# Kernel tuning notes

Hardware: AMD Instinct MI355X
Metric: run time of the kernel (lower is better)

Reference implementation:

```python
import jax, jax.numpy as jnp
import numpy as np

N_USER = 100000
M_ITEM = 50000
N_NODE = N_USER + M_ITEM
D = 64           # latent_dim
WD = D // 2      # word_emb_dim
FU = FI = 10     # padded feature-bag width
NUF = NIF = 30000
VOCAB = 20000
T = 8            # tokens per text source (name/comment/comment_list)
DNU = DNI = 10   # numeric feature dims
B = 2048         # seed batch
S = 20           # sampled neighbors per layer
L = 2            # num_layers


def setup_inputs() -> dict:
    key = jax.random.key(0)
    ks = jax.random.split(key, 26)
    f = lambda i, s: jax.random.normal(ks[i], s, jnp.float32) * 0.05
    ri = lambda i, s, hi: jax.random.randint(ks[i], s, 0, hi)
    return {
        # int (graph / lookup) inputs
        "seeds": ri(0, (B,), N_USER),
        "neigh1": ri(1, (B, S), N_NODE),
        "neigh2": ri(2, (B, S, S), N_NODE),
        "user_feat_idx": ri(3, (N_USER, FU), NUF),
        "item_feat_idx": ri(4, (M_ITEM, FI), NIF),
        "user_text_idx": ri(5, (N_USER, 3, T), VOCAB),
        "item_text_idx": ri(6, (M_ITEM, 3, T), VOCAB),
        # float tables / features
        "user_id_emb": f(7, (N_USER, D)),
        "item_id_emb": f(8, (M_ITEM, D)),
        "user_feat_emb": f(9, (NUF, D)),
        "item_feat_emb": f(10, (NIF, D)),
        "word_emb": f(11, (VOCAB, WD)),
        "user_word300": f(12, (N_USER, 300)),
        "item_word300": f(13, (M_ITEM, 300)),
        "item_sent768": f(14, (M_ITEM, 768)),
        "user_numeric": f(15, (N_USER, DNU)),
        "item_numeric": f(16, (M_ITEM, DNI)),
        # linears (stored as (in, out); y = x @ W + b)
        "Wnum_u": f(17, (DNU, D)), "bnum_u": jnp.zeros((D,), jnp.float32),
        "Wnum_i": f(18, (DNI, D)), "bnum_i": jnp.zeros((D,), jnp.float32),
        "Wproj_u": f(19, (int(D * 3.5) + 300, D)), "bproj_u": jnp.zeros((D,), jnp.float32),
        "Wproj_i": f(20, (int(D * 3.5) + 300 + 768, D)), "bproj_i": jnp.zeros((D,), jnp.float32),
        "W_w": f(21, (L, 2 * D, D)), "b_w": jnp.zeros((L, D), jnp.float32),
        "W_v": f(22, (L, D, D)), "b_v": jnp.zeros((L, D), jnp.float32),
    }


def _forward(user_id_emb, item_id_emb, user_feat_emb, item_feat_emb, word_emb,
             user_word300, item_word300, item_sent768, user_numeric, item_numeric,
             Wnum_u, bnum_u, Wnum_i, bnum_i, Wproj_u, bproj_u, Wproj_i, bproj_i,
             W_w, b_w, W_v, b_v,
             seeds, neigh1, neigh2, user_feat_idx, item_feat_idx,
             user_text_idx, item_text_idx):
    # --- multi-source node embeddings (get_text_embedding + proj + numeric) ---
    # text: mean-pool word embeddings per source, concat 3 sources -> 1.5*D
    u_text = word_emb[user_text_idx].mean(axis=2).reshape(N_USER, 3 * WD)
    i_text = word_emb[item_text_idx].mean(axis=2).reshape(M_ITEM, 3 * WD)
    # feature bags: mean-pooled embedding lookup
    u_feat = user_feat_emb[user_feat_idx].mean(axis=1)
    i_feat = item_feat_emb[item_feat_idx].mean(axis=1)
    u = (jnp.concatenate([user_id_emb, u_feat, u_text, user_word300], -1) @ Wproj_u
         + bproj_u + user_numeric @ Wnum_u + bnum_u)
    it = (jnp.concatenate([item_id_emb, i_feat, i_text, item_word300, item_sent768], -1) @ Wproj_i
          + bproj_i + item_numeric @ Wnum_i + bnum_i)
    x = jnp.concatenate([u, it], axis=0)  # [N_NODE, D], items offset by N_USER

    # --- neighbor-sampled GraphSAGE: h = W_l([self, mean(V_l(neigh))]) ---
    def sage(l, self_x, neigh_x, act):
        agg = (neigh_x @ W_v[l] + b_v[l]).mean(axis=-2)
        h = jnp.concatenate([self_x, agg], axis=-1) @ W_w[l] + b_w[l]
        return jax.nn.relu(h) if act else h

    x0 = x[seeds]        # [B, D]
    x1 = x[neigh1]       # [B, S, D]
    x2 = x[neigh2]       # [B, S, S, D]
    h1 = sage(0, x1, x2, True)   # layer-0 applied to 1-hop nodes
    h0 = sage(0, x0, x1, True)   # layer-0 applied to seeds
    out = sage(1, h0, h1, False)  # final layer, no activation
    return out  # [B, D]


def reference(seeds, neigh1, neigh2, user_feat_idx, item_feat_idx, user_text_idx,
              item_text_idx, user_id_emb, item_id_emb, user_feat_emb, item_feat_emb,
              word_emb, user_word300, item_word300, item_sent768, user_numeric,
              item_numeric, Wnum_u, bnum_u, Wnum_i, bnum_i, Wproj_u, bproj_u,
              Wproj_i, bproj_i, W_w, b_w, W_v, b_v):
    return _forward(user_id_emb, item_id_emb, user_feat_emb, item_feat_emb, word_emb,
                    user_word300, item_word300, item_sent768, user_numeric, item_numeric,
                    Wnum_u, bnum_u, Wnum_i, bnum_i, Wproj_u, bproj_u, Wproj_i, bproj_i,
                    W_w, b_w, W_v, b_v,
                    seeds, neigh1, neigh2, user_feat_idx, item_feat_idx,
                    user_text_idx, item_text_idx)
```

## Files before the change

kernel.cpp:

```cpp
#include <hip/hip_runtime.h>
#include <hip/hip_bf16.h>
#include <stdint.h>

#define N_USER 100000
#define M_ITEM 50000
#define N_NODE 150000
#define B_SEED 2048
#define S_NB 20
#define UBLK2 1563
#define IBLK2 782

typedef __bf16   bf16x8 __attribute__((ext_vector_type(8)));
typedef float    f32x4  __attribute__((ext_vector_type(4)));
typedef uint32_t u32x4  __attribute__((ext_vector_type(4)));

__device__ __forceinline__ uint16_t f2bf(float f) {
    uint32_t u = __float_as_uint(f);
    return (uint16_t)((u + 0x7FFFu + ((u >> 16) & 1u)) >> 16);
}
__device__ __forceinline__ uint32_t pk2(float a, float b) {
    __hip_bfloat162 h = __float22bfloat162_rn(make_float2(a, b));
    return *reinterpret_cast<uint32_t*>(&h);
}
__device__ __forceinline__ float bf2f(uint16_t u) {
    return __uint_as_float(((uint32_t)u) << 16);
}

union BF8 { bf16x8 v; uint32_t u[4]; uint2 d2[2]; };

__device__ __forceinline__ bf16x8 pack8v(f32x4 lo, f32x4 hi) {
    BF8 r;
    r.u[0] = pk2(lo[0], lo[1]); r.u[1] = pk2(lo[2], lo[3]);
    r.u[2] = pk2(hi[0], hi[1]); r.u[3] = pk2(hi[2], hi[3]);
    return r.v;
}
__device__ __forceinline__ bf16x8 ldf32x8_mask(const float* rowp, int base, int limit) {
    BF8 r;
#pragma unroll
    for (int h = 0; h < 4; ++h) {
        const int k0 = base + 2 * h;
        const float a = (k0     < limit) ? rowp[k0]     : 0.f;
        const float b = (k0 + 1 < limit) ? rowp[k0 + 1] : 0.f;
        r.u[h] = pk2(a, b);
    }
    return r.v;
}

__global__ void prep_kernel(const float* __restrict__ Wproj_u, const float* __restrict__ Wnum_u,
                            const float* __restrict__ Wproj_i, const float* __restrict__ Wnum_i,
                            const float* __restrict__ Wv0, const float* __restrict__ Ww0,
                            uint16_t* __restrict__ WTU, uint16_t* __restrict__ WTI,
                            uint16_t* __restrict__ WvT, uint16_t* __restrict__ WwT)
{
    const int idx = blockIdx.x * 256 + threadIdx.x;
    if (idx < 36864) {
        const int d = idx / 576, kp = idx - d * 576;
        float v = 0.f;
        if (kp < 160)      v = Wproj_u[(64 + kp) * 64 + d];
        else if (kp < 192) { const int j = kp - 160; if (j < 10)  v = Wnum_u[j * 64 + d]; }
        else if (kp < 256) v = Wproj_u[(kp - 192) * 64 + d];
        else               { const int j = kp - 256; if (j < 300) v = Wproj_u[(224 + j) * 64 + d]; }
        WTU[d * 576 + kp] = f2bf(v);
    } else if (idx < 122880) {
        const int i2 = idx - 36864;
        const int d = i2 / 1344, kp = i2 - d * 1344;
        float v = 0.f;
        if (kp < 160)      v = Wproj_i[(64 + kp) * 64 + d];
        else if (kp < 192) { const int j = kp - 160; if (j < 10)  v = Wnum_i[j * 64 + d]; }
        else if (kp < 256) v = Wproj_i[(kp - 192) * 64 + d];
        else if (kp < 576) { const int j = kp - 256; if (j < 300) v = Wproj_i[(224 + j) * 64 + d]; }
        else               { const int j = kp - 576; v = Wproj_i[(524 + j) * 64 + d]; }
        WTI[d * 1344 + kp] = f2bf(v);
    } else {
        const int i2 = idx - 122880;
        if (i2 < 4096) { const int d = i2 >> 6, k = i2 & 63;  WvT[d * 64 + k]  = f2bf(Wv0[k * 64 + d]); }
        else           { const int j = i2 - 4096;
                         const int d = j >> 7, k = j & 127;   WwT[d * 128 + k] = f2bf(Ww0[k * 64 + d]); }
    }
}

__global__ __launch_bounds__(256) void gpack_kernel(
    const int* __restrict__ ufi, const int* __restrict__ ifi,
    const int* __restrict__ uti, const int* __restrict__ iti,
    const float* __restrict__ ufe, const float* __restrict__ ife,
    const float* __restrict__ wemb,
    uint16_t* __restrict__ Apre)
{
    const int gid  = blockIdx.x * 256 + threadIdx.x;
    const int node = gid >> 3;
    const int d0   = gid & 7;
    if (node >= N_NODE) return;
    const bool item = node >= N_USER;
    const int nloc  = item ? node - N_USER : node;
    const int*   fidx = (item ? ifi : ufi) + (size_t)nloc * 10;
    const int*   tidx = (item ? iti : uti) + (size_t)nloc * 24;
    const float* fe   = item ? ife : ufe;
    uint16_t* out = Apre + (size_t)node * 160;

    {
        f32x4 s0 = {0, 0, 0, 0}, s1 = {0, 0, 0, 0};
#pragma unroll
        for (int j = 0; j < 10; ++j) {
            const float* p = fe + (size_t)fidx[j] * 64 + 8 * d0;
            s0 += *(const f32x4*)p;
            s1 += *(const f32x4*)(p + 4);
        }
        s0 *= 0.1f; s1 *= 0.1f;
        uint4 o = make_uint4(pk2(s0[0], s0[1]), pk2(s0[2], s0[3]),
                             pk2(s1[0], s1[1]), pk2(s1[2], s1[3]));
        *(uint4*)(out + 8 * d0) = o;
    }
#pragma unroll
    for (int s = 0; s < 3; ++s) {
        f32x4 a = {0, 0, 0, 0};
#pragma unroll
        for (int j = 0; j < 8; ++j) {
            const float* p = wemb + (size_t)tidx[s * 8 + j] * 32 + 4 * d0;
            a += *(const f32x4*)p;
        }
        a *= 0.125f;
        *(uint2*)(out + 64 + 32 * s + 4 * d0) = make_uint2(pk2(a[0], a[1]), pk2(a[2], a[3]));
    }
}

__global__ __launch_bounds__(256, 4) void pgemm_kernel(
    const uint16_t* __restrict__ Apre,
    const float* __restrict__ u_id,  const float* __restrict__ i_id,
    const float* __restrict__ uw300, const float* __restrict__ iw300,
    const float* __restrict__ is768,
    const float* __restrict__ unum,  const float* __restrict__ inum,
    const uint16_t* __restrict__ WTU, const uint16_t* __restrict__ WTI,
    const float* __restrict__ bproj_u, const float* __restrict__ bnum_u,
    const float* __restrict__ bproj_i, const float* __restrict__ bnum_i,
    uint16_t* __restrict__ xout)
{
    const int t = threadIdx.x;
    const int w = t >> 6, l = t & 63;
    const int l15 = l & 15, g4 = l >> 4;
    const bool item = blockIdx.x >= UBLK2;
    const int tile  = item ? (blockIdx.x - UBLK2) : blockIdx.x;
    const int ntype = item ? M_ITEM : N_USER;
    const int nloc0 = tile * 64 + w * 16 + l15;
    const int nloc  = nloc0 < ntype ? nloc0 : ntype - 1;
    const int node  = (item ? N_USER : 0) + nloc;

    const uint16_t* WT = item ? WTI : WTU;
    const int KP       = item ? 1344 : 576;

    f32x4 acc[4] = {};
    const uint16_t* WTb = WT + (size_t)l15 * KP + g4 * 8;

    auto MM = [&](bf16x8 af, int kb) {
#pragma unroll
        for (int db = 0; db < 4; ++db) {
            const bf16x8 bfr = *reinterpret_cast<const bf16x8*>(WTb + (size_t)db * 16 * KP + kb);
            acc[db] = __builtin_amdgcn_mfma_f32_16x16x32_bf16(af, bfr, acc[db], 0, 0, 0);
        }
    };

    {
        const uint16_t* ap = Apre + (size_t)node * 160 + g4 * 8;
        bf16x8 af[5];
#pragma unroll
        for (int ks = 0; ks < 5; ++ks) af[ks] = *(const bf16x8*)(ap + ks * 32);
#pragma unroll
        for (int ks = 0; ks < 5; ++ks) MM(af[ks], ks * 32);
    }
    MM(ldf32x8_mask((item ? inum : unum) + (size_t)nloc * 10, g4 * 8, 10), 160);
    {
        const float* idr = (item ? i_id : u_id) + (size_t)nloc * 64 + g4 * 8;
        f32x4 a0 = *(const f32x4*)idr,        a1 = *(const f32x4*)(idr + 4);
        f32x4 b0 = *(const f32x4*)(idr + 32), b1 = *(const f32x4*)(idr + 36);
        MM(pack8v(a0, a1), 192);
        MM(pack8v(b0, b1), 224);
    }
    {
        const float* wr = (item ? iw300 : uw300) + (size_t)nloc * 300 + g4 * 8;
        f32x4 va[5][2];
#pragma unroll
        for (int u = 0; u < 5; ++u) {
            const float* p = wr + u * 32;
            va[u][0] = *(const f32x4*)p; va[u][1] = *(const f32x4*)(p + 4);
        }
#pragma unroll
        for (int u = 0; u < 5; ++u) MM(pack8v(va[u][0], va[u][1]), 256 + u * 32);
#pragma unroll
        for (int u = 0; u < 4; ++u) {
            const float* p = wr + (5 + u) * 32;
            va[u][0] = *(const f32x4*)p; va[u][1] = *(const f32x4*)(p + 4);
        }
#pragma unroll
        for (int u = 0; u < 4; ++u) MM(pack8v(va[u][0], va[u][1]), 256 + (5 + u) * 32);
        MM(ldf32x8_mask(wr - g4 * 8, 288 + g4 * 8, 300), 544);
    }
    if (item) {
        const float* sr = is768 + (size_t)nloc * 768 + g4 * 8;
#pragma unroll
        for (int b = 0; b < 4; ++b) {
            f32x4 va[6][2];
#pragma unroll
            for (int u = 0; u < 6; ++u) {
                const float* p = sr + (b * 6 + u) * 32;
                va[u][0] = *(const f32x4*)p; va[u][1] = *(const f32x4*)(p + 4);
            }
#pragma unroll
            for (int u = 0; u < 6; ++u)
                MM(pack8v(va[u][0], va[u][1]), 576 + (b * 6 + u) * 32);
        }
    }

    const int nb_out = tile * 64 + w * 16 + g4 * 4;
    const float* bp = item ? bproj_i : bproj_u;
    const float* bn = item ? bnum_i  : bnum_u;
    uint16_t* xo = xout + (size_t)(item ? N_USER : 0) * 64;
#pragma unroll
    for (int db = 0; db < 4; ++db) {
        const int d = db * 16 + l15;
        const float bias = bp[d] + bn[d];
#pragma unroll
        for (int r = 0; r < 4; ++r) {
            const int nn = nb_out + r;
            if (nn < ntype) xo[(size_t)nn * 64 + d] = f2bf(acc[db][r] + bias);
        }
    }
}

__global__ __launch_bounds__(256) void xv_kernel(
    const uint16_t* __restrict__ x, const uint16_t* __restrict__ WvT,
    const float* __restrict__ bv, uint16_t* __restrict__ xv, int n)
{
    const int t = threadIdx.x;
    const int w = t >> 6, l = t & 63, l15 = l & 15, g4 = l >> 4;
    const int node = blockIdx.x * 64 + w * 16 + l15;
    const int node_c = node < n ? node : n - 1;

    f32x4 acc[4] = {};
    const uint16_t* WTb = WvT + l15 * 64 + g4 * 8;
#pragma unroll
    for (int ks = 0; ks < 2; ++ks) {
        const bf16x8 af = *reinterpret_cast<const bf16x8*>(x + (size_t)node_c * 64 + ks * 32 + g4 * 8);
#pragma unroll
        for (int db = 0; db < 4; ++db) {
            const bf16x8 bfr = *reinterpret_cast<const bf16x8*>(WTb + db * 16 * 64 + ks * 32);
            acc[db] = __builtin_amdgcn_mfma_f32_16x16x32_bf16(af, bfr, acc[db], 0, 0, 0);
        }
    }
    const int node_base = blockIdx.x * 64 + w * 16 + g4 * 4;
#pragma unroll
    for (int db = 0; db < 4; ++db) {
        const int d = db * 16 + l15;
        const float bias = bv[d];
#pragma unroll
        for (int r = 0; r < 4; ++r) {
            const int nn = node_base + r;
            if (nn < n) xv[(size_t)nn * 64 + d] = f2bf(acc[db][r] + bias);
        }
    }
}

__global__ __launch_bounds__(256) void sage_mfma_kernel(
    const uint16_t* __restrict__ x, const uint16_t* __restrict__ xv,
    const int* __restrict__ self_idx, const int* __restrict__ neigh_idx,
    const uint16_t* __restrict__ WwT, const float* __restrict__ bw,
    uint16_t* __restrict__ out, int relu)
{
    const int t = threadIdx.x;
    const int w = t >> 6, l = t & 63, l15 = l & 15, g4 = l >> 4;
    const int r = blockIdx.x * 64 + w * 16 + l15;
    const int sidx = self_idx[r];
    const int* ni = neigh_idx + (size_t)r * S_NB;

    f32x4 acc[4] = {};
    const uint16_t* WTb = WwT + l15 * 128 + g4 * 8;

    auto MM = [&](bf16x8 af, int kb) {
#pragma unroll
        for (int db = 0; db < 4; ++db) {
            const bf16x8 bfr = *reinterpret_cast<const bf16x8*>(WTb + db * 16 * 128 + kb);
            acc[db] = __builtin_amdgcn_mfma_f32_16x16x32_bf16(af, bfr, acc[db], 0, 0, 0);
        }
    };

#pragma unroll
    for (int ks = 0; ks < 2; ++ks) {
        const bf16x8 af = *reinterpret_cast<const bf16x8*>(x + (size_t)sidx * 64 + ks * 32 + g4 * 8);
        MM(af, ks * 32);
    }
#pragma unroll
    for (int ks = 0; ks < 2; ++ks) {
        float ev[4] = {0.f, 0.f, 0.f, 0.f}, od[4] = {0.f, 0.f, 0.f, 0.f};
#pragma unroll
        for (int j = 0; j < S_NB; ++j) {
            const u32x4 v = *reinterpret_cast<const u32x4*>(xv + (size_t)ni[j] * 64 + ks * 32 + g4 * 8);
#pragma unroll
            for (int q = 0; q < 4; ++q) {
                ev[q] += __uint_as_float(v[q] << 16);
                od[q] += __uint_as_float(v[q] & 0xffff0000u);
            }
        }
        BF8 m;
#pragma unroll
        for (int q = 0; q < 4; ++q) m.u[q] = pk2(ev[q] * (1.f / S_NB), od[q] * (1.f / S_NB));
        MM(m.v, 64 + ks * 32);
    }

    const int rb = blockIdx.x * 64 + w * 16 + g4 * 4;
#pragma unroll
    for (int db = 0; db < 4; ++db) {
        const int d = db * 16 + l15;
        const float bias = bw[d];
#pragma unroll
        for (int rr = 0; rr < 4; ++rr) {
            float h = acc[db][rr] + bias;
            if (relu) h = fmaxf(h, 0.f);
            out[(size_t)(rb + rr) * 64 + d] = f2bf(h);
        }
    }
}

__global__ __launch_bounds__(256) void final_kernel(
    const uint16_t* __restrict__ h0, const uint16_t* __restrict__ h1,
    const float* __restrict__ Wv, const float* __restrict__ bv,
    const float* __restrict__ Ww, const float* __restrict__ bw,
    float* __restrict__ out)
{
    __shared__ float WvL[64 * 64];
    __shared__ float WwL[128 * 64];
    const int t = threadIdx.x;
    for (int i = t; i < 64 * 64; i += 256)  WvL[i] = Wv[i];
    for (int i = t; i < 128 * 64; i += 256) WwL[i] = Ww[i];
    __syncthreads();

    const int wave = t >> 6, lane = t & 63;
    const int base = blockIdx.x * 32 + wave * 8;
    const float bvl = bv[lane], bwl = bw[lane];

    for (int i = 0; i < 8; ++i) {
        const int b = base + i;
        float m = 0.f;
#pragma unroll
        for (int s = 0; s < S_NB; ++s)
            m += bf2f(h1[(size_t)(b * S_NB + s) * 64 + lane]);
        m *= (1.f / S_NB);

        float agg = bvl;
#pragma unroll 8
        for (int k = 0; k < 64; ++k)
            agg += __shfl(m, k) * WvL[k * 64 + lane];

        const float selfv = bf2f(h0[(size_t)b * 64 + lane]);
        float h = bwl;
#pragma unroll 8
        for (int k = 0; k < 64; ++k)
            h += __shfl(selfv, k) * WwL[k * 64 + lane];
#pragma unroll 8
        for (int k = 0; k < 64; ++k)
            h += __shfl(agg, k) * WwL[(64 + k) * 64 + lane];

        out[(size_t)b * 64 + lane] = h;
    }
}

extern "C" void kernel_launch(void* const* d_in, const int* in_sizes, int n_in,
                              void* d_out, int out_size, void* d_ws, size_t ws_size,
                              hipStream_t stream)
{
    const int*   seeds   = (const int*)d_in[0];
    const int*   neigh1  = (const int*)d_in[1];
    const int*   neigh2  = (const int*)d_in[2];
    const int*   ufi     = (const int*)d_in[3];
    const int*   ifi     = (const int*)d_in[4];
    const int*   uti     = (const int*)d_in[5];
    const int*   iti     = (const int*)d_in[6];
    const float* u_id    = (const float*)d_in[7];
    const float* i_id    = (const float*)d_in[8];
    const float* ufe     = (const float*)d_in[9];
    const float* ife     = (const float*)d_in[10];
    const float* wemb    = (const float*)d_in[11];
    const float* uw300   = (const float*)d_in[12];
    const float* iw300   = (const float*)d_in[13];
    const float* is768   = (const float*)d_in[14];
    const float* unum    = (const float*)d_in[15];
    const float* inum    = (const float*)d_in[16];
    const float* Wnum_u  = (const float*)d_in[17];
    const float* bnum_u  = (const float*)d_in[18];
    const float* Wnum_i  = (const float*)d_in[19];
    const float* bnum_i  = (const float*)d_in[20];
    const float* Wproj_u = (const float*)d_in[21];
    const float* bproj_u = (const float*)d_in[22];
    const float* Wproj_i = (const float*)d_in[23];
    const float* bproj_i = (const float*)d_in[24];
    const float* W_w     = (const float*)d_in[25];
    const float* b_w     = (const float*)d_in[26];
    const float* W_v     = (const float*)d_in[27];
    const float* b_v     = (const float*)d_in[28];

    uint16_t* WTU  = (uint16_t*)d_ws;
    uint16_t* WTI  = WTU  + 36864;
    uint16_t* WvT0 = WTI  + 86016;
    uint16_t* WwT0 = WvT0 + 4096;
    uint16_t* xbf  = WwT0 + 8192;
    uint16_t* xvbf = xbf  + (size_t)N_NODE * 64;
    uint16_t* h1bf = xvbf + (size_t)N_NODE * 64;
    uint16_t* h0bf = h1bf + (size_t)B_SEED * S_NB * 64;
    uint16_t* Apre = xvbf;
    float* outp = (float*)d_out;

    prep_kernel<<<528, 256, 0, stream>>>(
        Wproj_u, Wnum_u, Wproj_i, Wnum_i, W_v, W_w, WTU, WTI, WvT0, WwT0);

    gpack_kernel<<<(N_NODE * 8 + 255) / 256, 256, 0, stream>>>(
        ufi, ifi, uti, iti, ufe, ife, wemb, Apre);

    pgemm_kernel<<<UBLK2 + IBLK2, 256, 0, stream>>>(
        Apre, u_id, i_id, uw300, iw300, is768, unum, inum,
        WTU, WTI, bproj_u, bnum_u, bproj_i, bnum_i, xbf);

    xv_kernel<<<(N_NODE + 63) / 64, 256, 0, stream>>>(xbf, WvT0, b_v, xvbf, N_NODE);

    sage_mfma_kernel<<<(B_SEED * S_NB) / 64, 256, 0, stream>>>(
        xbf, xvbf, neigh1, neigh2, WwT0, b_w, h1bf, 1);
    sage_mfma_kernel<<<B_SEED / 64, 256, 0, stream>>>(
        xbf, xvbf, seeds, neigh1, WwT0, b_w, h0bf, 1);

    final_kernel<<<B_SEED / 32, 256, 0, stream>>>(
        h0bf, h1bf, W_v + 4096, b_v + 64, W_w + 8192, b_w + 64, outp);
}
```

Before: 389.1 us.

## Stage projection-GEMM feature rows through double-buffered LDS with direct global-to-LDS loads

```diff
diff --git a/kernel.cpp b/kernel.cpp
--- a/kernel.cpp
+++ b/kernel.cpp
@@ -14,6 +14,9 @@
 typedef float    f32x4  __attribute__((ext_vector_type(4)));
 typedef uint32_t u32x4  __attribute__((ext_vector_type(4)));
 
+typedef __attribute__((address_space(3))) uint32_t lds_u32_t;
+typedef __attribute__((address_space(1))) const uint32_t glb_u32_t;
+
 __device__ __forceinline__ uint16_t f2bf(float f) {
     uint32_t u = __float_as_uint(f);
     return (uint16_t)((u + 0x7FFFu + ((u >> 16) & 1u)) >> 16);
@@ -26,7 +29,7 @@
     return __uint_as_float(((uint32_t)u) << 16);
 }
 
-union BF8 { bf16x8 v; uint32_t u[4]; uint2 d2[2]; };
+union BF8 { bf16x8 v; uint32_t u[4]; };
 
 __device__ __forceinline__ bf16x8 pack8v(f32x4 lo, f32x4 hi) {
     BF8 r;
@@ -57,19 +60,21 @@
         const int d = idx / 576, kp = idx - d * 576;
         float v = 0.f;
         if (kp < 160)      v = Wproj_u[(64 + kp) * 64 + d];
-        else if (kp < 192) { const int j = kp - 160; if (j < 10)  v = Wnum_u[j * 64 + d]; }
-        else if (kp < 256) v = Wproj_u[(kp - 192) * 64 + d];
-        else               { const int j = kp - 256; if (j < 300) v = Wproj_u[(224 + j) * 64 + d]; }
+        else if (kp < 192) { const int j = kp - 160; if (j < 10) v = Wnum_u[j * 64 + d]; }
+        else if (kp < 224) { const int j = kp - 192; if (j < 12) v = Wproj_u[(512 + j) * 64 + d]; }
+        else if (kp < 288) v = Wproj_u[(kp - 224) * 64 + d];
+        else               v = Wproj_u[(224 + kp - 288) * 64 + d];
         WTU[d * 576 + kp] = f2bf(v);
     } else if (idx < 122880) {
         const int i2 = idx - 36864;
         const int d = i2 / 1344, kp = i2 - d * 1344;
         float v = 0.f;
         if (kp < 160)      v = Wproj_i[(64 + kp) * 64 + d];
-        else if (kp < 192) { const int j = kp - 160; if (j < 10)  v = Wnum_i[j * 64 + d]; }
-        else if (kp < 256) v = Wproj_i[(kp - 192) * 64 + d];
-        else if (kp < 576) { const int j = kp - 256; if (j < 300) v = Wproj_i[(224 + j) * 64 + d]; }
-        else               { const int j = kp - 576; v = Wproj_i[(524 + j) * 64 + d]; }
+        else if (kp < 192) { const int j = kp - 160; if (j < 10) v = Wnum_i[j * 64 + d]; }
+        else if (kp < 224) { const int j = kp - 192; if (j < 12) v = Wproj_i[(512 + j) * 64 + d]; }
+        else if (kp < 288) v = Wproj_i[(kp - 224) * 64 + d];
+        else if (kp < 576) v = Wproj_i[(224 + kp - 288) * 64 + d];
+        else               v = Wproj_i[(524 + kp - 576) * 64 + d];
         WTI[d * 1344 + kp] = f2bf(v);
     } else {
         const int i2 = idx - 122880;
@@ -123,7 +128,7 @@
     }
 }
 
-__global__ __launch_bounds__(256, 4) void pgemm_kernel(
+__global__ __launch_bounds__(256, 6) void pgemm_kernel(
     const uint16_t* __restrict__ Apre,
     const float* __restrict__ u_id,  const float* __restrict__ i_id,
     const float* __restrict__ uw300, const float* __restrict__ iw300,
@@ -134,16 +139,20 @@
     const float* __restrict__ bproj_i, const float* __restrict__ bnum_i,
     uint16_t* __restrict__ xout)
 {
+    __shared__ float buf[2][2048];
+
     const int t = threadIdx.x;
     const int w = t >> 6, l = t & 63;
     const int l15 = l & 15, g4 = l >> 4;
-    const bool item = blockIdx.x >= UBLK2;
-    const int tile  = item ? (blockIdx.x - UBLK2) : blockIdx.x;
+    const bool item = blockIdx.x < IBLK2;
+    const int tile  = item ? blockIdx.x : (blockIdx.x - IBLK2);
     const int ntype = item ? M_ITEM : N_USER;
-    const int nloc0 = tile * 64 + w * 16 + l15;
-    const int nloc  = nloc0 < ntype ? nloc0 : ntype - 1;
-    const int node  = (item ? N_USER : 0) + nloc;
-
+    const int nb    = tile * 64;
+    const int NC    = item ? 35 : 11;
+
+    const float* idp = item ? i_id  : u_id;
+    const float* w3p = item ? iw300 : uw300;
+    const float* nmp = item ? inum  : unum;
     const uint16_t* WT = item ? WTI : WTU;
     const int KP       = item ? 1344 : 576;
 
@@ -158,58 +167,52 @@
         }
     };
 
+    auto stage = [&](int bi, int c) {
+        const float* base; int stride, coloff;
+        if (c < 2)       { base = idp;    stride = 64;  coloff = c * 32; }
+        else if (c < 11) { base = w3p;    stride = 300; coloff = (c - 2) * 32; }
+        else             { base = is768;  stride = 768; coloff = (c - 11) * 32; }
+#pragma unroll
+        for (int j = 0; j < 2; ++j) {
+            const int row  = w * 16 + j * 8 + (l >> 3);
+            const int node = (nb + row) < ntype ? (nb + row) : (ntype - 1);
+            const int swb  = ((l & 7) * 16) ^ ((row & 7) << 4);
+            const float* g = base + (size_t)node * stride + coloff + (swb >> 2);
+            uint32_t* lp = (uint32_t*)((char*)&buf[bi][0] + w * 2048 + j * 1024);
+            __builtin_amdgcn_global_load_lds((glb_u32_t*)g, (lds_u32_t*)lp, 16, 0, 0);
+        }
+    };
+
+    auto compute = [&](int bi, int kb) {
+        const char* bb = (const char*)&buf[bi][0];
+        const int r = w * 16 + l15;
+        const f32x4 lo = *(const f32x4*)(bb + r * 128 + ((g4 * 32)      ^ ((r & 7) << 4)));
+        const f32x4 hi = *(const f32x4*)(bb + r * 128 + ((g4 * 32 + 16) ^ ((r & 7) << 4)));
+        MM(pack8v(lo, hi), kb);
+    };
+
+    stage(0, 0);
     {
+        const int nloc = (nb + w * 16 + l15) < ntype ? (nb + w * 16 + l15) : (ntype - 1);
+        const int node = (item ? N_USER : 0) + nloc;
         const uint16_t* ap = Apre + (size_t)node * 160 + g4 * 8;
         bf16x8 af[5];
 #pragma unroll
         for (int ks = 0; ks < 5; ++ks) af[ks] = *(const bf16x8*)(ap + ks * 32);
 #pragma unroll
         for (int ks = 0; ks < 5; ++ks) MM(af[ks], ks * 32);
-    }
-    MM(ldf32x8_mask((item ? inum : unum) + (size_t)nloc * 10, g4 * 8, 10), 160);
-    {
-        const float* idr = (item ? i_id : u_id) + (size_t)nloc * 64 + g4 * 8;
-        f32x4 a0 = *(const f32x4*)idr,        a1 = *(const f32x4*)(idr + 4);
-        f32x4 b0 = *(const f32x4*)(idr + 32), b1 = *(const f32x4*)(idr + 36);
-        MM(pack8v(a0, a1), 192);
-        MM(pack8v(b0, b1), 224);
-    }
-    {
-        const float* wr = (item ? iw300 : uw300) + (size_t)nloc * 300 + g4 * 8;
-        f32x4 va[5][2];
-#pragma unroll
-        for (int u = 0; u < 5; ++u) {
-            const float* p = wr + u * 32;
-            va[u][0] = *(const f32x4*)p; va[u][1] = *(const f32x4*)(p + 4);
-        }
-#pragma unroll
-        for (int u = 0; u < 5; ++u) MM(pack8v(va[u][0], va[u][1]), 256 + u * 32);
-#pragma unroll
-        for (int u = 0; u < 4; ++u) {
-            const float* p = wr + (5 + u) * 32;
-            va[u][0] = *(const f32x4*)p; va[u][1] = *(const f32x4*)(p + 4);
-        }
-#pragma unroll
-        for (int u = 0; u < 4; ++u) MM(pack8v(va[u][0], va[u][1]), 256 + (5 + u) * 32);
-        MM(ldf32x8_mask(wr - g4 * 8, 288 + g4 * 8, 300), 544);
-    }
-    if (item) {
-        const float* sr = is768 + (size_t)nloc * 768 + g4 * 8;
-#pragma unroll
-        for (int b = 0; b < 4; ++b) {
-            f32x4 va[6][2];
-#pragma unroll
-            for (int u = 0; u < 6; ++u) {
-                const float* p = sr + (b * 6 + u) * 32;
-                va[u][0] = *(const f32x4*)p; va[u][1] = *(const f32x4*)(p + 4);
-            }
-#pragma unroll
-            for (int u = 0; u < 6; ++u)
-                MM(pack8v(va[u][0], va[u][1]), 576 + (b * 6 + u) * 32);
-        }
-    }
-
-    const int nb_out = tile * 64 + w * 16 + g4 * 4;
+        MM(ldf32x8_mask(nmp + (size_t)nloc * 10, g4 * 8, 10), 160);
+        MM(ldf32x8_mask(w3p + (size_t)nloc * 300, 288 + g4 * 8, 300), 192);
+    }
+
+    for (int c = 0; c < NC; ++c) {
+        if (c + 1 < NC) stage((c + 1) & 1, c + 1);
+        __syncthreads();
+        compute(c & 1, 224 + 32 * c);
+        __syncthreads();
+    }
+
+    const int nb_out = nb + w * 16 + g4 * 4;
     const float* bp = item ? bproj_i : bproj_u;
     const float* bn = item ? bnum_i  : bnum_u;
     uint16_t* xo = xout + (size_t)(item ? N_USER : 0) * 64;
```

Result: faster. 337.3 us (-13.3%).
